# Optimization experiments

Hardware: AMD Instinct MI355X
Metric: run time of the kernel (lower is better)

Reference implementation:

```python
import jax, jax.numpy as jnp
import numpy as np

N = 50000       # nodes
E = 800000      # edges (avg degree 16)
IN_F = 128
OUT_F = 128
NEG_SLOPE = 0.2  # LeakyReLU alpha
EPS = 1e-10


def setup_inputs() -> dict:
    key = jax.random.key(0)
    k1, k2, k3, k4 = jax.random.split(key, 4)
    h = jax.random.normal(k1, (N, IN_F), dtype=jnp.float32)
    edge_index = jax.random.randint(k2, (2, E), 0, N, dtype=jnp.int32)
    # nn.Linear(in, out, bias=False): weight is [out, in], Wh = h @ W.T
    W = jax.random.normal(k3, (OUT_F, IN_F), dtype=jnp.float32) * (1.0 / np.sqrt(IN_F))
    # a: [2*out, 1], xavier_uniform with gain=1.414
    lim = 1.414 * np.sqrt(6.0 / (2 * OUT_F + 1))
    a = jax.random.uniform(k4, (2 * OUT_F, 1), dtype=jnp.float32, minval=-lim, maxval=lim)
    return {"h": h, "edge_index": edge_index, "W": W, "a": a}


def reference(h, edge_index, W, a):
    Wh = h @ W.T                              # [N, out]
    rows = edge_index[0]
    cols = edge_index[1]
    # cat([Wh_i, Wh_j],1) @ a  ==  (Wh @ a1)[rows] + (Wh @ a2)[cols]
    a1 = a[:OUT_F, 0]
    a2 = a[OUT_F:, 0]
    s1 = Wh @ a1                              # [N]
    s2 = Wh @ a2                              # [N]
    e = jax.nn.leaky_relu(s1[rows] + s2[cols], negative_slope=NEG_SLOPE)  # [E]
    e = e - jnp.max(e)
    exp_e = jnp.exp(e)
    sum_exp = jax.ops.segment_sum(exp_e, rows, num_segments=N)            # [N]
    alpha = exp_e / (sum_exp[rows] + EPS)                                 # [E]
    # sparse.mm(adj_att, Wh): h_prime[i] = sum_j alpha_ij * Wh[j]
    h_prime = jax.ops.segment_sum(alpha[:, None] * Wh[cols], rows, num_segments=N)
    return jax.nn.elu(h_prime)
```

## Files before the change

### kernel.cpp

```cpp
#include <hip/hip_runtime.h>

constexpr int FD = 128;
constexpr int NBMAX = 512;
constexpr int CH1 = 2048;
constexpr int CAPB = 3072;

typedef __attribute__((ext_vector_type(8))) short short8;
typedef __attribute__((ext_vector_type(4))) float floatx4;

__device__ __forceinline__ unsigned fenc(float f) {
    unsigned u = __float_as_uint(f);
    return (u & 0x80000000u) ? ~u : (u | 0x80000000u);
}
__device__ __forceinline__ float fdec(unsigned e) {
    return (e & 0x80000000u) ? __uint_as_float(e & 0x7fffffffu)
                             : __uint_as_float(~e);
}

__device__ __forceinline__ unsigned bpack(float x, float y) {
    unsigned ux = __float_as_uint(x); ux += 0x7FFFu + ((ux >> 16) & 1u);
    unsigned uy = __float_as_uint(y); uy += 0x7FFFu + ((uy >> 16) & 1u);
    return (ux >> 16) | (uy & 0xFFFF0000u);
}

__global__ __launch_bounds__(128) void initwt_kernel(const float* __restrict__ W,
                                                     unsigned* __restrict__ Wb,
                                                     int* __restrict__ bcursor,
                                                     unsigned* __restrict__ maxslot) {
    int j = blockIdx.x, k = threadIdx.x;
    float w = W[(size_t)j * FD + k];
    float pw = __shfl_xor(w, 1, 64);
    if ((k & 1) == 0) Wb[(size_t)j * 64 + (k >> 1)] = bpack(w, pw);
    if (j == 0) {
        for (int i = k; i < NBMAX; i += 128) bcursor[i] = 0;
        if (k < 2) maxslot[k] = 0x007FFFFFu;
    }
}

union GBShared {
    struct {
        int cnt[NBMAX];
        int ex[NBMAX];
        int gbase[NBMAX];
        int wtot[8];
        unsigned stage[CH1];
    } bin;
    struct {
        float m1[8];
        float m2[8];
    } gm;
};

__global__ __launch_bounds__(512) void gembin_kernel(const float* __restrict__ h,
                                                     const unsigned* __restrict__ Wb,
                                                     const float* __restrict__ a,
                                                     const int* __restrict__ ei,
                                                     int* __restrict__ bcursor,
                                                     unsigned* __restrict__ Whb,
                                                     float* __restrict__ s1,
                                                     float* __restrict__ s2,
                                                     unsigned* __restrict__ ebuf,
                                                     unsigned* __restrict__ maxslot,
                                                     int n, int e_cnt, int ngemm) {
    __shared__ GBShared sh;
    int t = threadIdx.x;

    if ((int)blockIdx.x < ngemm) {
        int w = t >> 6, lane = t & 63;
        int quad = lane >> 4, c = lane & 15;
        int rbase = blockIdx.x * 128 + w * 16;

        int arow = min(rbase + c, n - 1);
        const float4* hrow = (const float4*)(h + (size_t)arow * FD);
        union { uint4 u; short8 s; } af[4];
#pragma unroll
        for (int kk = 0; kk < 4; ++kk) {
            int k0 = kk * 32 + quad * 8;
            float4 f0 = hrow[k0 >> 2];
            float4 f1 = hrow[(k0 >> 2) + 1];
            af[kk].u.x = bpack(f0.x, f0.y);
            af[kk].u.y = bpack(f0.z, f0.w);
            af[kk].u.z = bpack(f1.x, f1.y);
            af[kk].u.w = bpack(f1.z, f1.w);
        }

        float p1a[4] = {0.f, 0.f, 0.f, 0.f};
        float p2a[4] = {0.f, 0.f, 0.f, 0.f};

#pragma unroll
        for (int tt = 0; tt < 8; ++tt) {
            const uint4* brow = (const uint4*)(Wb + (size_t)(tt * 16 + c) * 64 + quad * 4);
            floatx4 acc = {0.f, 0.f, 0.f, 0.f};
#pragma unroll
            for (int kk = 0; kk < 4; ++kk) {
                union { uint4 u; short8 s; } bf;
                bf.u = brow[kk * 4];
                acc = __builtin_amdgcn_mfma_f32_16x16x32_bf16(af[kk].s, bf.s, acc, 0, 0, 0);
            }
            float a1v = a[tt * 16 + c];
            float a2v = a[FD + tt * 16 + c];
#pragma unroll
            for (int i = 0; i < 4; ++i) {
                float v = acc[i];
                p1a[i] = fmaf(v, a1v, p1a[i]);
                p2a[i] = fmaf(v, a2v, p2a[i]);
                float pv = __shfl_xor(v, 1, 64);
                int r = rbase + quad * 4 + i;
                if ((c & 1) == 0 && r < n)
                    Whb[(size_t)r * 64 + tt * 8 + (c >> 1)] = bpack(v, pv);
            }
        }

#pragma unroll
        for (int d = 1; d < 16; d <<= 1) {
#pragma unroll
            for (int i = 0; i < 4; ++i) {
                p1a[i] += __shfl_xor(p1a[i], d, 64);
                p2a[i] += __shfl_xor(p2a[i], d, 64);
            }
        }
        if (c == 0) {
#pragma unroll
            for (int i = 0; i < 4; ++i) {
                int r = rbase + quad * 4 + i;
                if (r < n) { s1[r] = p1a[i]; s2[r] = p2a[i]; }
            }
        }

        float m1 = -3.0e38f, m2 = -3.0e38f;
#pragma unroll
        for (int i = 0; i < 4; ++i) {
            int r = rbase + quad * 4 + i;
            if (r < n) { m1 = fmaxf(m1, p1a[i]); m2 = fmaxf(m2, p2a[i]); }
        }
        m1 = fmaxf(m1, __shfl_xor(m1, 16, 64));
        m1 = fmaxf(m1, __shfl_xor(m1, 32, 64));
        m2 = fmaxf(m2, __shfl_xor(m2, 16, 64));
        m2 = fmaxf(m2, __shfl_xor(m2, 32, 64));
        if (lane == 0) { sh.gm.m1[w] = m1; sh.gm.m2[w] = m2; }
        __syncthreads();
        if (t == 0) {
            float g1 = -3.0e38f, g2 = -3.0e38f;
#pragma unroll
            for (int k = 0; k < 8; ++k) {
                g1 = fmaxf(g1, sh.gm.m1[k]);
                g2 = fmaxf(g2, sh.gm.m2[k]);
            }
            atomicMax(&maxslot[0], fenc(g1));
            atomicMax(&maxslot[1], fenc(g2));
        }
    } else {
        int bb = blockIdx.x - ngemm;
        sh.bin.cnt[t] = 0;
        __syncthreads();
        int base = bb * CH1;
        int m = min(CH1, e_cnt - base);

        unsigned pack[4];
        int rank[4], bkt[4];
        int nk = 0;
#pragma unroll
        for (int k = 0; k < 4; ++k) {
            int idx = t + k * 512;
            if (idx < m) {
                int ed = base + idx;
                int r = ei[ed];
                int cc = ei[e_cnt + ed];
                unsigned p = ((unsigned)r << 16) | (unsigned)cc;
                int b = r >> 7;
                pack[nk] = p;
                bkt[nk] = b;
                rank[nk] = atomicAdd(&sh.bin.cnt[b], 1);
                ++nk;
            }
        }
        __syncthreads();

        int l = t & 63, w = t >> 6;
        int v = sh.bin.cnt[t];
        int iv = v;
#pragma unroll
        for (int d = 1; d < 64; d <<= 1) {
            int u = __shfl_up(iv, d, 64);
            if (l >= d) iv += u;
        }
        if (l == 63) sh.bin.wtot[w] = iv;
        __syncthreads();
        if (t == 0) {
            int s = 0;
#pragma unroll
            for (int k = 0; k < 8; ++k) { int x = sh.bin.wtot[k]; sh.bin.wtot[k] = s; s += x; }
        }
        __syncthreads();
        int excl = iv - v + sh.bin.wtot[w];
        sh.bin.ex[t] = excl;
        if (v > 0) sh.bin.gbase[t] = atomicAdd(&bcursor[t], v);
        __syncthreads();
        for (int k = 0; k < nk; ++k)
            sh.bin.stage[sh.bin.ex[bkt[k]] + rank[k]] = pack[k];
        __syncthreads();
        for (int s = t; s < m; s += 512) {
            unsigned p = sh.bin.stage[s];
            int b = p >> 23;
            int pos = sh.bin.gbase[b] + (s - sh.bin.ex[b]);
            if (pos < CAPB) ebuf[(size_t)b * CAPB + pos] = p;
        }
    }
}

__global__ __launch_bounds__(1024) void agg_kernel(const unsigned* __restrict__ ebuf,
                                                   const int* __restrict__ bcnt,
                                                   const float* __restrict__ s1,
                                                   const float* __restrict__ s2,
                                                   const unsigned* __restrict__ Whb,
                                                   const unsigned* __restrict__ maxslot,
                                                   float* __restrict__ out, int n) {
    __shared__ uint2 pairs[CAPB];
    __shared__ int cnt[128];
    __shared__ int exs[128];
    __shared__ float invs[128];
    __shared__ float s1l[128];
    int b = blockIdx.x;
    int t = threadIdx.x;
    int row0 = b << 7;
    int m = min(bcnt[b], CAPB);

    if (t < 128) {
        cnt[t] = 0;
        int gr = row0 + t;
        s1l[t] = (gr < n) ? s1[gr] : 0.f;
    }
    __syncthreads();

    unsigned pk[3];
    int rk[3], lrr[3];
    int nk = 0;
#pragma unroll
    for (int k = 0; k < 3; ++k) {
        int idx = t + (k << 10);
        if (idx < m) {
            unsigned p = ebuf[(size_t)b * CAPB + idx];
            int lr = (p >> 16) & 127;
            pk[nk] = p;
            lrr[nk] = lr;
            rk[nk] = atomicAdd(&cnt[lr], 1);
            ++nk;
        }
    }
    __syncthreads();

    if (t < 64) {
        int va = cnt[t], vb = cnt[t + 64];
        int ia = va, ib = vb;
#pragma unroll
        for (int d = 1; d < 64; d <<= 1) {
            int ua = __shfl_up(ia, d, 64);
            int ub = __shfl_up(ib, d, 64);
            if (t >= d) { ia += ua; ib += ub; }
        }
        int tot = __shfl(ia, 63, 64);
        exs[t] = ia - va;
        exs[t + 64] = tot + ib - vb;
    }
    __syncthreads();

    float M = fdec(maxslot[0]) + fdec(maxslot[1]);
    M = (M >= 0.f) ? M : 0.2f * M;

    for (int k = 0; k < nk; ++k) {
        unsigned p = pk[k];
        int col = p & 0xFFFF;
        float sv = s1l[lrr[k]] + s2[col];
        float le = (sv >= 0.f) ? sv : 0.2f * sv;
        float ev = expf(le - M);
        pairs[exs[lrr[k]] + rk[k]] = make_uint2((unsigned)col, __float_as_uint(ev));
    }
    __syncthreads();

    {
        int hw = t >> 5, fl = t & 31;
        for (int r = hw; r < 128; r += 32) {
            int s0 = exs[r], d = cnt[r];
            float s = 0.f;
            for (int k2 = fl; k2 < d; k2 += 32)
                s += __uint_as_float(pairs[s0 + k2].y);
#pragma unroll
            for (int dd = 1; dd < 32; dd <<= 1)
                s += __shfl_xor(s, dd, 64);
            if (fl == 0) invs[r] = 1.0f / (s + 1e-10f);
        }
    }
    __syncthreads();

    int w = t >> 6, l = t & 63, half = l >> 5, fl = l & 31;
    for (int ni = (w << 3); ni < (w << 3) + 8; ++ni) {
        int node = row0 + ni;
        if (node >= n) break;
        int s0 = exs[ni], deg = cnt[ni];
        float4 acc = make_float4(0.f, 0.f, 0.f, 0.f);
        int j = half;
        for (; j + 2 < deg; j += 4) {
            uint2 q0 = pairs[s0 + j];
            uint2 q1 = pairs[s0 + j + 2];
            float a0 = __uint_as_float(q0.y), a1 = __uint_as_float(q1.y);
            uint2 b0 = *(const uint2*)(Whb + (size_t)q0.x * 64 + 2 * fl);
            uint2 b1 = *(const uint2*)(Whb + (size_t)q1.x * 64 + 2 * fl);
            acc.x = fmaf(a0, __uint_as_float(b0.x << 16), acc.x);
            acc.y = fmaf(a0, __uint_as_float(b0.x & 0xFFFF0000u), acc.y);
            acc.z = fmaf(a0, __uint_as_float(b0.y << 16), acc.z);
            acc.w = fmaf(a0, __uint_as_float(b0.y & 0xFFFF0000u), acc.w);
            acc.x = fmaf(a1, __uint_as_float(b1.x << 16), acc.x);
            acc.y = fmaf(a1, __uint_as_float(b1.x & 0xFFFF0000u), acc.y);
            acc.z = fmaf(a1, __uint_as_float(b1.y << 16), acc.z);
            acc.w = fmaf(a1, __uint_as_float(b1.y & 0xFFFF0000u), acc.w);
        }
        if (j < deg) {
            uint2 q0 = pairs[s0 + j];
            float a0 = __uint_as_float(q0.y);
            uint2 b0 = *(const uint2*)(Whb + (size_t)q0.x * 64 + 2 * fl);
            acc.x = fmaf(a0, __uint_as_float(b0.x << 16), acc.x);
            acc.y = fmaf(a0, __uint_as_float(b0.x & 0xFFFF0000u), acc.y);
            acc.z = fmaf(a0, __uint_as_float(b0.y << 16), acc.z);
            acc.w = fmaf(a0, __uint_as_float(b0.y & 0xFFFF0000u), acc.w);
        }
        acc.x += __shfl_xor(acc.x, 32, 64);
        acc.y += __shfl_xor(acc.y, 32, 64);
        acc.z += __shfl_xor(acc.z, 32, 64);
        acc.w += __shfl_xor(acc.w, 32, 64);
        if (half == 0) {
            float inv = invs[ni];
            float x = acc.x * inv, y = acc.y * inv, z = acc.z * inv, u = acc.w * inv;
            float4 r;
            r.x = (x > 0.f) ? x : expm1f(x);
            r.y = (y > 0.f) ? y : expm1f(y);
            r.z = (z > 0.f) ? z : expm1f(z);
            r.w = (u > 0.f) ? u : expm1f(u);
            ((float4*)(out + (size_t)node * FD))[fl] = r;
        }
    }
}

extern "C" void kernel_launch(void* const* d_in, const int* in_sizes, int n_in,
                              void* d_out, int out_size, void* d_ws, size_t ws_size,
                              hipStream_t stream) {
    const float* h = (const float*)d_in[0];
    const int* ei  = (const int*)d_in[1];
    const float* W = (const float*)d_in[2];
    const float* a = (const float*)d_in[3];
    float* out = (float*)d_out;
    int n = in_sizes[0] / FD;
    int e = in_sizes[1] / 2;
    int nb = (n + 127) >> 7;

    char* ws = (char*)d_ws;
    size_t off = 0;
    auto alloc = [&](size_t bytes) -> void* {
        void* p = ws + off;
        off += bytes;
        off = (off + 255) & ~(size_t)255;
        return p;
    };
    unsigned* Whb     = (unsigned*)alloc((size_t)n * 64 * sizeof(unsigned));
    unsigned* Wb      = (unsigned*)alloc((size_t)FD * 64 * sizeof(unsigned));
    float*    s1      = (float*)alloc((size_t)n * sizeof(float));
    float*    s2      = (float*)alloc((size_t)n * sizeof(float));
    int*      bcursor = (int*)alloc((size_t)NBMAX * sizeof(int));
    unsigned* ebuf    = (unsigned*)alloc((size_t)NBMAX * CAPB * sizeof(unsigned));
    unsigned* maxslot = (unsigned*)alloc(2 * sizeof(unsigned));

    int ngemm = (n + 127) / 128;
    int nbin = (e + CH1 - 1) / CH1;

    initwt_kernel<<<FD, 128, 0, stream>>>(W, Wb, bcursor, maxslot);
    gembin_kernel<<<ngemm + nbin, 512, 0, stream>>>(h, Wb, a, ei, bcursor, Whb,
                                                    s1, s2, ebuf, maxslot, n, e, ngemm);
    agg_kernel<<<nb, 1024, 0, stream>>>(ebuf, bcursor, s1, s2, Whb, maxslot, out, n);
}
```

Before: 145.0 us.

## Transpose MFMA operands for row-contiguous Wh stores and widen aggregation gathers

The GEMM stage swaps the MFMA operand order so each lane holds four consecutive output features of one node. That lets it write Wh as packed 8-byte stores per node and compute s1/s2 with fewer shuffles. The aggregation stage now gathers 16-byte bf16 chunks, with 16 lanes per edge and 4 edges in flight per wave instead of 8-byte chunks over 2 edges, and adds a wider cross-lane reduction. It also prefetches s2 during the binning pass and uses the fast __expf, which slightly lowers precision.

```diff
diff --git a/kernel.cpp b/kernel.cpp
--- a/kernel.cpp
+++ b/kernel.cpp
@@ -69,74 +69,59 @@
         int w = t >> 6, lane = t & 63;
         int quad = lane >> 4, c = lane & 15;
         int rbase = blockIdx.x * 128 + w * 16;
-
-        int arow = min(rbase + c, n - 1);
+        int node = rbase + c;
+
+        int arow = min(node, n - 1);
         const float4* hrow = (const float4*)(h + (size_t)arow * FD);
-        union { uint4 u; short8 s; } af[4];
+        union { uint4 u; short8 s; } hf[4];
 #pragma unroll
         for (int kk = 0; kk < 4; ++kk) {
             int k0 = kk * 32 + quad * 8;
             float4 f0 = hrow[k0 >> 2];
             float4 f1 = hrow[(k0 >> 2) + 1];
-            af[kk].u.x = bpack(f0.x, f0.y);
-            af[kk].u.y = bpack(f0.z, f0.w);
-            af[kk].u.z = bpack(f1.x, f1.y);
-            af[kk].u.w = bpack(f1.z, f1.w);
-        }
-
-        float p1a[4] = {0.f, 0.f, 0.f, 0.f};
-        float p2a[4] = {0.f, 0.f, 0.f, 0.f};
+            hf[kk].u.x = bpack(f0.x, f0.y);
+            hf[kk].u.y = bpack(f0.z, f0.w);
+            hf[kk].u.z = bpack(f1.x, f1.y);
+            hf[kk].u.w = bpack(f1.z, f1.w);
+        }
+
+        float p1 = 0.f, p2 = 0.f;
 
 #pragma unroll
         for (int tt = 0; tt < 8; ++tt) {
-            const uint4* brow = (const uint4*)(Wb + (size_t)(tt * 16 + c) * 64 + quad * 4);
+            const uint4* wrow = (const uint4*)(Wb + (size_t)(tt * 16 + c) * 64 + quad * 4);
             floatx4 acc = {0.f, 0.f, 0.f, 0.f};
 #pragma unroll
             for (int kk = 0; kk < 4; ++kk) {
-                union { uint4 u; short8 s; } bf;
-                bf.u = brow[kk * 4];
-                acc = __builtin_amdgcn_mfma_f32_16x16x32_bf16(af[kk].s, bf.s, acc, 0, 0, 0);
+                union { uint4 u; short8 s; } wf;
+                wf.u = wrow[kk * 4];
+                acc = __builtin_amdgcn_mfma_f32_16x16x32_bf16(wf.s, hf[kk].s, acc, 0, 0, 0);
             }
-            float a1v = a[tt * 16 + c];
-            float a2v = a[FD + tt * 16 + c];
-#pragma unroll
-            for (int i = 0; i < 4; ++i) {
-                float v = acc[i];
-                p1a[i] = fmaf(v, a1v, p1a[i]);
-                p2a[i] = fmaf(v, a2v, p2a[i]);
-                float pv = __shfl_xor(v, 1, 64);
-                int r = rbase + quad * 4 + i;
-                if ((c & 1) == 0 && r < n)
-                    Whb[(size_t)r * 64 + tt * 8 + (c >> 1)] = bpack(v, pv);
+            float4 a1q = *(const float4*)(a + tt * 16 + quad * 4);
+            float4 a2q = *(const float4*)(a + FD + tt * 16 + quad * 4);
+            p1 = fmaf(acc[0], a1q.x, p1); p1 = fmaf(acc[1], a1q.y, p1);
+            p1 = fmaf(acc[2], a1q.z, p1); p1 = fmaf(acc[3], a1q.w, p1);
+            p2 = fmaf(acc[0], a2q.x, p2); p2 = fmaf(acc[1], a2q.y, p2);
+            p2 = fmaf(acc[2], a2q.z, p2); p2 = fmaf(acc[3], a2q.w, p2);
+            if (node < n) {
+                uint2 pk2;
+                pk2.x = bpack(acc[0], acc[1]);
+                pk2.y = bpack(acc[2], acc[3]);
+                *(uint2*)(Whb + (size_t)node * 64 + tt * 8 + quad * 2) = pk2;
             }
         }
 
+        p1 += __shfl_xor(p1, 16, 64); p1 += __shfl_xor(p1, 32, 64);
+        p2 += __shfl_xor(p2, 16, 64); p2 += __shfl_xor(p2, 32, 64);
+        if (quad == 0 && node < n) { s1[node] = p1; s2[node] = p2; }
+
+        float m1 = (node < n) ? p1 : -3.0e38f;
+        float m2 = (node < n) ? p2 : -3.0e38f;
 #pragma unroll
         for (int d = 1; d < 16; d <<= 1) {
-#pragma unroll
-            for (int i = 0; i < 4; ++i) {
-                p1a[i] += __shfl_xor(p1a[i], d, 64);
-                p2a[i] += __shfl_xor(p2a[i], d, 64);
-            }
-        }
-        if (c == 0) {
-#pragma unroll
-            for (int i = 0; i < 4; ++i) {
-                int r = rbase + quad * 4 + i;
-                if (r < n) { s1[r] = p1a[i]; s2[r] = p2a[i]; }
-            }
-        }
-
-        float m1 = -3.0e38f, m2 = -3.0e38f;
-#pragma unroll
-        for (int i = 0; i < 4; ++i) {
-            int r = rbase + quad * 4 + i;
-            if (r < n) { m1 = fmaxf(m1, p1a[i]); m2 = fmaxf(m2, p2a[i]); }
-        }
-        m1 = fmaxf(m1, __shfl_xor(m1, 16, 64));
-        m1 = fmaxf(m1, __shfl_xor(m1, 32, 64));
-        m2 = fmaxf(m2, __shfl_xor(m2, 16, 64));
-        m2 = fmaxf(m2, __shfl_xor(m2, 32, 64));
+            m1 = fmaxf(m1, __shfl_xor(m1, d, 64));
+            m2 = fmaxf(m2, __shfl_xor(m2, d, 64));
+        }
         if (lane == 0) { sh.gm.m1[w] = m1; sh.gm.m2[w] = m2; }
         __syncthreads();
         if (t == 0) {
@@ -207,6 +192,16 @@
         }
     }
 }
+
+#define FMA8(bv, av)                                                    \
+    acc[0] = fmaf(av, __uint_as_float((bv).x << 16), acc[0]);           \
+    acc[1] = fmaf(av, __uint_as_float((bv).x & 0xFFFF0000u), acc[1]);   \
+    acc[2] = fmaf(av, __uint_as_float((bv).y << 16), acc[2]);           \
+    acc[3] = fmaf(av, __uint_as_float((bv).y & 0xFFFF0000u), acc[3]);   \
+    acc[4] = fmaf(av, __uint_as_float((bv).z << 16), acc[4]);           \
+    acc[5] = fmaf(av, __uint_as_float((bv).z & 0xFFFF0000u), acc[5]);   \
+    acc[6] = fmaf(av, __uint_as_float((bv).w << 16), acc[6]);           \
+    acc[7] = fmaf(av, __uint_as_float((bv).w & 0xFFFF0000u), acc[7]);
 
 __global__ __launch_bounds__(1024) void agg_kernel(const unsigned* __restrict__ ebuf,
                                                    const int* __restrict__ bcnt,
@@ -234,6 +229,7 @@
 
     unsigned pk[3];
     int rk[3], lrr[3];
+    float s2v[3];
     int nk = 0;
 #pragma unroll
     for (int k = 0; k < 3; ++k) {
@@ -243,6 +239,7 @@
             int lr = (p >> 16) & 127;
             pk[nk] = p;
             lrr[nk] = lr;
+            s2v[nk] = s2[p & 0xFFFFu];
             rk[nk] = atomicAdd(&cnt[lr], 1);
             ++nk;
         }
@@ -269,11 +266,10 @@
 
     for (int k = 0; k < nk; ++k) {
         unsigned p = pk[k];
-        int col = p & 0xFFFF;
-        float sv = s1l[lrr[k]] + s2[col];
+        float sv = s1l[lrr[k]] + s2v[k];
         float le = (sv >= 0.f) ? sv : 0.2f * sv;
-        float ev = expf(le - M);
-        pairs[exs[lrr[k]] + rk[k]] = make_uint2((unsigned)col, __float_as_uint(ev));
+        float ev = __expf(le - M);
+        pairs[exs[lrr[k]] + rk[k]] = make_uint2(p & 0xFFFFu, __float_as_uint(ev));
     }
     __syncthreads();
 
@@ -292,50 +288,46 @@
     }
     __syncthreads();
 
-    int w = t >> 6, l = t & 63, half = l >> 5, fl = l & 31;
+    int w = t >> 6, l = t & 63, q = l >> 4, fl2 = l & 15;
     for (int ni = (w << 3); ni < (w << 3) + 8; ++ni) {
         int node = row0 + ni;
         if (node >= n) break;
         int s0 = exs[ni], deg = cnt[ni];
-        float4 acc = make_float4(0.f, 0.f, 0.f, 0.f);
-        int j = half;
-        for (; j + 2 < deg; j += 4) {
-            uint2 q0 = pairs[s0 + j];
-            uint2 q1 = pairs[s0 + j + 2];
-            float a0 = __uint_as_float(q0.y), a1 = __uint_as_float(q1.y);
-            uint2 b0 = *(const uint2*)(Whb + (size_t)q0.x * 64 + 2 * fl);
-            uint2 b1 = *(const uint2*)(Whb + (size_t)q1.x * 64 + 2 * fl);
-            acc.x = fmaf(a0, __uint_as_float(b0.x << 16), acc.x);
-            acc.y = fmaf(a0, __uint_as_float(b0.x & 0xFFFF0000u), acc.y);
-            acc.z = fmaf(a0, __uint_as_float(b0.y << 16), acc.z);
-            acc.w = fmaf(a0, __uint_as_float(b0.y & 0xFFFF0000u), acc.w);
-            acc.x = fmaf(a1, __uint_as_float(b1.x << 16), acc.x);
-            acc.y = fmaf(a1, __uint_as_float(b1.x & 0xFFFF0000u), acc.y);
-            acc.z = fmaf(a1, __uint_as_float(b1.y << 16), acc.z);
-            acc.w = fmaf(a1, __uint_as_float(b1.y & 0xFFFF0000u), acc.w);
+        float acc[8] = {0.f, 0.f, 0.f, 0.f, 0.f, 0.f, 0.f, 0.f};
+        int j = q;
+        for (; j + 4 < deg; j += 8) {
+            uint2 e0 = pairs[s0 + j];
+            uint2 e1 = pairs[s0 + j + 4];
+            uint4 b0 = *(const uint4*)(Whb + (size_t)e0.x * 64 + 4 * fl2);
+            uint4 b1 = *(const uint4*)(Whb + (size_t)e1.x * 64 + 4 * fl2);
+            float a0 = __uint_as_float(e0.y);
+            float a1 = __uint_as_float(e1.y);
+            FMA8(b0, a0)
+            FMA8(b1, a1)
         }
         if (j < deg) {
-            uint2 q0 = pairs[s0 + j];
-            float a0 = __uint_as_float(q0.y);
-            uint2 b0 = *(const uint2*)(Whb + (size_t)q0.x * 64 + 2 * fl);
-            acc.x = fmaf(a0, __uint_as_float(b0.x << 16), acc.x);
-            acc.y = fmaf(a0, __uint_as_float(b0.x & 0xFFFF0000u), acc.y);
-            acc.z = fmaf(a0, __uint_as_float(b0.y << 16), acc.z);
-            acc.w = fmaf(a0, __uint_as_float(b0.y & 0xFFFF0000u), acc.w);
-        }
-        acc.x += __shfl_xor(acc.x, 32, 64);
-        acc.y += __shfl_xor(acc.y, 32, 64);
-        acc.z += __shfl_xor(acc.z, 32, 64);
-        acc.w += __shfl_xor(acc.w, 32, 64);
-        if (half == 0) {
+            uint2 e0 = pairs[s0 + j];
+            uint4 b0 = *(const uint4*)(Whb + (size_t)e0.x * 64 + 4 * fl2);
+            float a0 = __uint_as_float(e0.y);
+            FMA8(b0, a0)
+        }
+#pragma unroll
+        for (int i = 0; i < 8; ++i) {
+            acc[i] += __shfl_xor(acc[i], 16, 64);
+            acc[i] += __shfl_xor(acc[i], 32, 64);
+        }
+        if (q < 2) {
             float inv = invs[ni];
-            float x = acc.x * inv, y = acc.y * inv, z = acc.z * inv, u = acc.w * inv;
+            float v0 = (q ? acc[4] : acc[0]) * inv;
+            float v1 = (q ? acc[5] : acc[1]) * inv;
+            float v2 = (q ? acc[6] : acc[2]) * inv;
+            float v3 = (q ? acc[7] : acc[3]) * inv;
             float4 r;
-            r.x = (x > 0.f) ? x : expm1f(x);
-            r.y = (y > 0.f) ? y : expm1f(y);
-            r.z = (z > 0.f) ? z : expm1f(z);
-            r.w = (u > 0.f) ? u : expm1f(u);
-            ((float4*)(out + (size_t)node * FD))[fl] = r;
+            r.x = (v0 > 0.f) ? v0 : expm1f(v0);
+            r.y = (v1 > 0.f) ? v1 : expm1f(v1);
+            r.z = (v2 > 0.f) ? v2 : expm1f(v2);
+            r.w = (v3 > 0.f) ? v3 : expm1f(v3);
+            *((float4*)(out + (size_t)node * FD + fl2 * 8 + q * 4)) = r;
         }
     }
 }
```

Result: no change. 145.1 us (+0.1%).
